# Optimization experiments

Hardware: AMD Instinct MI355X
Metric: run time of the kernel (lower is better)

Reference implementation:

```python
import jax, jax.numpy as jnp
import numpy as np

N = 200000
B = 2
GX, GY, GZ = 480, 360, 32          # full-res voxel grid for input_coords
GX2, GY2, GZ2 = 240, 180, 16       # output_scale grid for bxyz_indx
CIN, CR, COUT = 64, 64, 64
CR2 = CR // 2
P_SCALE = (2, 4, 6, 8)


def setup_inputs() -> dict:
    key = jax.random.key(0)
    ks = jax.random.split(key, 24)
    s = 0.05
    input_data = jax.random.normal(ks[0], (N, CIN), dtype=jnp.float32)
    bcol = jax.random.randint(ks[1], (N, 1), 0, B, dtype=jnp.int32)
    xc = jax.random.randint(ks[2], (N, 1), 0, GX, dtype=jnp.int32)
    yc = jax.random.randint(ks[3], (N, 1), 0, GY, dtype=jnp.int32)
    zc = jax.random.randint(ks[4], (N, 1), 0, GZ, dtype=jnp.int32)
    input_coords = jnp.concatenate([bcol, xc, yc, zc], axis=1)
    input_coords_inv = jax.random.randint(ks[5], (N,), 0, N, dtype=jnp.int32)
    b2 = jax.random.randint(ks[6], (N, 1), 0, B, dtype=jnp.int32)
    x2 = jax.random.randint(ks[7], (N, 1), 0, GX2, dtype=jnp.int32)
    y2 = jax.random.randint(ks[8], (N, 1), 0, GY2, dtype=jnp.int32)
    z2 = jax.random.randint(ks[9], (N, 1), 0, GZ2, dtype=jnp.int32)
    bxyz_indx = jnp.concatenate([b2, x2, y2, z2], axis=1)
    # parameters (torch Linear stored here as [in, out])
    W_red = jax.random.normal(ks[10], (CIN, CR)) * s
    b_red = jnp.zeros((CR,), jnp.float32)
    fc_list_W = jax.random.normal(ks[11], (4, CR, CR2)) * s
    fc_list_b = jnp.zeros((4, CR2), jnp.float32)
    fcs_W = jax.random.normal(ks[12], (4, CR2, CR2)) * s
    fcs_b = jnp.zeros((4, CR2), jnp.float32)
    fc_W = jax.random.normal(ks[13], (CR2, CR2)) * s
    out_fc_W = jax.random.normal(ks[14], (CR2, CR)) * s
    lo_W1 = jax.random.normal(ks[15], (2 * CR, CR)) * s
    lo_W2 = jax.random.normal(ks[16], (CR, COUT)) * s
    lo_b2 = jnp.zeros((COUT,), jnp.float32)
    return dict(input_data=input_data, input_coords=input_coords,
                input_coords_inv=input_coords_inv, bxyz_indx=bxyz_indx,
                W_red=W_red, b_red=b_red, fc_list_W=fc_list_W, fc_list_b=fc_list_b,
                fcs_W=fcs_W, fcs_b=fcs_b, fc_W=fc_W, out_fc_W=out_fc_W,
                lo_W1=lo_W1, lo_W2=lo_W2, lo_b2=lo_b2)


def _segment_mean(x, seg, num_segments):
    sums = jax.ops.segment_sum(x, seg, num_segments=num_segments)
    cnt = jax.ops.segment_sum(jnp.ones((x.shape[0], 1), x.dtype), seg,
                              num_segments=num_segments)
    return sums / jnp.maximum(cnt, 1.0)


def reference(input_data, input_coords, input_coords_inv, bxyz_indx,
              W_red, b_red, fc_list_W, fc_list_b, fcs_W, fcs_b,
              fc_W, out_fc_W, lo_W1, lo_W2, lo_b2):
    reduced = jax.nn.relu(input_data @ W_red + b_red)          # [N, CR]
    bcol = input_coords[:, 0]
    xyz = input_coords[:, 1:]
    outs = []
    for j, ps in enumerate(P_SCALE):
        dx = (GX - 1) // ps + 1
        dy = (GY - 1) // ps + 1
        dz = (GZ - 1) // ps + 1
        q = xyz // ps                                          # [N, 3]
        # dense linearized voxel id replaces torch.unique(return_inverse)
        lin = ((bcol * dx + q[:, 0]) * dy + q[:, 1]) * dz + q[:, 2]
        nseg = B * dx * dy * dz
        fkm = _segment_mean(reduced, lin, nseg)                # [nseg, CR]
        att = jax.nn.relu(fkm @ fc_list_W[j] + fc_list_b[j])   # [nseg, CR2]
        outs.append(att[lin])                                  # gather back [N, CR2]
    scale_features = jnp.stack(outs, axis=1)                   # [N, 4, CR2]
    feat_S = scale_features.sum(axis=1)                        # [N, CR2]
    feat_Z = jax.nn.relu(feat_S @ fc_W)                        # [N, CR2]
    att_v = jax.nn.sigmoid(jnp.einsum('nc,kcd->nkd', feat_Z, fcs_W) + fcs_b)
    fused = (scale_features * att_v).sum(axis=1) @ out_fc_W    # [N, CR]
    output_f = jnp.concatenate([reduced, fused], axis=1)       # [N, 2*CR]
    proj = jax.nn.relu(output_f @ lo_W1) @ lo_W2 + lo_b2       # [N, COUT]
    proj = proj[input_coords_inv]
    # with_fm branch: index = (b, z, y, x) of bxyz_indx (b,x,y,z)
    lin2 = ((bxyz_indx[:, 0] * GZ2 + bxyz_indx[:, 3]) * GY2
            + bxyz_indx[:, 2]) * GX2 + bxyz_indx[:, 1]
    tv_fmap = jax.ops.segment_max(proj, lin2, num_segments=B * GZ2 * GY2 * GX2)
    tv_fmap = jnp.where(jnp.isneginf(tv_fmap), 0.0, tv_fmap)   # empty voxels -> 0
    return proj, tv_fmap, lin2
```

## Files before the change

kernel.cpp:

```cpp
#include <hip/hip_runtime.h>
#include <math.h>

#define NPTS   200000
#define CR     64
#define CR2    32

#define NSEG0      1382400
#define SUM123_ROW2 172800
#define SUM123_ROW3 230400
#define SUM123_ROWS 252000

#define TVSEG  1382400
#define GX2    240
#define GY2    180
#define GZ2    16

#define NBATCH 21600

__device__ __forceinline__ float bcastf(float v, int l) {
    return __int_as_float(__builtin_amdgcn_readlane(__float_as_int(v), l));
}

__device__ __forceinline__ int lin_scale(int b, int x, int y, int z,
                                         int ps, int dx, int dy, int dz) {
    int qx = x / ps, qy = y / ps, qz = z / ps;
    return ((b * dx + qx) * dy + qy) * dz + qz;
}

__device__ __forceinline__ void seg_decode(int seg, int& l1, int& l2, int& l3) {
    int qz = seg & 15; int rest = seg >> 4;
    int qy = rest % 180; int rest2 = rest / 180;
    int qx = rest2 % 240; int bb = rest2 / 240;
    l1 = ((bb * 120 + (qx >> 1)) * 90 + (qy >> 1)) * 8 + (qz >> 1);
    l2 = ((bb *  80 + (qx / 3)) * 60 + (qy / 3)) * 6 + (qz / 3);
    l3 = ((bb *  60 + (qx >> 2)) * 45 + (qy >> 2)) * 4 + (qz >> 2);
}

__global__ __launch_bounds__(256) void k_redscat(
        const float* __restrict__ in, const int* __restrict__ coords,
        const float* __restrict__ Wred, const float* __restrict__ bred,
        float* __restrict__ red, float* __restrict__ sum0,
        float* __restrict__ cnt) {
    __shared__ float Wl[CR * CR];
    for (int i = threadIdx.x; i < CR * CR; i += blockDim.x) Wl[i] = Wred[i];
    __syncthreads();
    int lane = threadIdx.x & 63;
    float bl = bred[lane];
    int wid  = blockIdx.x * 4 + (threadIdx.x >> 6);
    int nw   = gridDim.x * 4;
    for (int p = wid; p < NPTS / 2; p += nw) {
        int r0 = 2 * p, r1 = r0 + 1;
        float x0 = in[(size_t)r0 * CR + lane];
        float x1 = in[(size_t)r1 * CR + lane];
        float acc0 = bl, acc1 = bl;
#pragma unroll
        for (int k = 0; k < CR; ++k) {
            float w = Wl[k * CR + lane];
            acc0 += bcastf(x0, k) * w;
            acc1 += bcastf(x1, k) * w;
        }
        acc0 = fmaxf(acc0, 0.f); acc1 = fmaxf(acc1, 0.f);
        red[(size_t)r0 * CR + lane] = acc0;
        red[(size_t)r1 * CR + lane] = acc1;
        int4 c0 = ((const int4*)coords)[r0];
        int4 c1 = ((const int4*)coords)[r1];
        int l0a = lin_scale(c0.x, c0.y, c0.z, c0.w, 2, 240, 180, 16);
        int l0b = lin_scale(c1.x, c1.y, c1.z, c1.w, 2, 240, 180, 16);
        atomicAdd(&sum0[(size_t)l0a * CR + lane], acc0);
        atomicAdd(&sum0[(size_t)l0b * CR + lane], acc1);
        if (lane == 0) {
            atomicAdd(&cnt[l0a], 1.0f);
            atomicAdd(&cnt[l0b], 1.0f);
        }
    }
}

__global__ __launch_bounds__(256) void k_buildlist(
        const float* __restrict__ cnt, int* __restrict__ list0,
        int* __restrict__ listCount, int* __restrict__ rankArr) {
    __shared__ int s_wavecnt[4];
    __shared__ int s_base;
    int lane = threadIdx.x & 63;
    int w = threadIdx.x >> 6;
    int batch0 = blockIdx.x * 80 + w * 20;
    int mycount = 0;
    for (int b = 0; b < 20; ++b) {
        float c = cnt[(batch0 + b) * 64 + lane];
        unsigned long long mask = __ballot(c > 0.f);
        mycount += __popcll(mask);
    }
    if (lane == 0) s_wavecnt[w] = mycount;
    __syncthreads();
    if (threadIdx.x == 0) {
        int tot = s_wavecnt[0] + s_wavecnt[1] + s_wavecnt[2] + s_wavecnt[3];
        s_base = atomicAdd(listCount, tot);
    }
    __syncthreads();
    int offset = s_base;
    for (int ww = 0; ww < w; ++ww) offset += s_wavecnt[ww];
    for (int b = 0; b < 20; ++b) {
        int cell = (batch0 + b) * 64 + lane;
        float c = cnt[cell];
        unsigned long long mask = __ballot(c > 0.f);
        if (c > 0.f) {
            int my = offset + __popcll(mask & ((1ull << lane) - 1ull));
            list0[my] = cell;
            rankArr[cell] = my;
        }
        offset += __popcll(mask);
    }
}

__global__ __launch_bounds__(256) void k_gatt(
        const float* __restrict__ sum0, float* __restrict__ attbuf,
        const float* __restrict__ cnt,
        const float* __restrict__ fcW, const float* __restrict__ fcB) {
    __shared__ float sw[3 * CR * CR2];
    for (int i = threadIdx.x; i < 3 * CR * CR2; i += blockDim.x)
        sw[i] = fcW[CR * CR2 + i];
    __syncthreads();
    int lane = threadIdx.x & 63;
    int d = lane & 31;
    int wid = blockIdx.x * 4 + (threadIdx.x >> 6);
    int nw  = gridDim.x * 4;
    for (int s = wid; s < SUM123_ROWS; s += nw) {
        int childLin = -1;
        const float* w; float bj;
        if (s < SUM123_ROW2) {
            int qz = s & 7, t = s >> 3;
            int qy = t % 90, t2 = t / 90;
            int qx = t2 % 120, b = t2 / 120;
            if (lane < 8) {
                int i = (lane >> 2) & 1, j = (lane >> 1) & 1, k = lane & 1;
                childLin = ((b * 240 + 2 * qx + i) * 180 + 2 * qy + j) * 16 + 2 * qz + k;
            }
            w = sw; bj = fcB[1 * CR2 + d];
        } else if (s < SUM123_ROW3) {
            int s2 = s - SUM123_ROW2;
            int qz = s2 % 6, t = s2 / 6;
            int qy = t % 60, t2 = t / 60;
            int qx = t2 % 80, b = t2 / 80;
            if (lane < 27) {
                int i = lane / 9, j = (lane / 3) % 3, k = lane % 3;
                int cz = 3 * qz + k;
                if (cz < 16)
                    childLin = ((b * 240 + 3 * qx + i) * 180 + 3 * qy + j) * 16 + cz;
            }
            w = sw + 2048; bj = fcB[2 * CR2 + d];
        } else {
            int s3 = s - SUM123_ROW3;
            int qz = s3 & 3, t = s3 >> 2;
            int qy = t % 45, t2 = t / 45;
            int qx = t2 % 60, b = t2 / 60;
            int i = lane >> 4, j = (lane >> 2) & 3, k = lane & 3;
            childLin = ((b * 240 + 4 * qx + i) * 180 + 4 * qy + j) * 16 + 4 * qz + k;
            w = sw + 4096; bj = fcB[3 * CR2 + d];
        }
        float myc = (childLin >= 0) ? cnt[childLin] : 0.f;
        unsigned long long mask = __ballot(myc > 0.f);
        if (!mask) continue;
        float ctot = myc;
        ctot += __shfl_xor(ctot, 1, 64);
        ctot += __shfl_xor(ctot, 2, 64);
        ctot += __shfl_xor(ctot, 4, 64);
        ctot += __shfl_xor(ctot, 8, 64);
        ctot += __shfl_xor(ctot, 16, 64);
        ctot += __shfl_xor(ctot, 32, 64);
        float acc = 0.f;
        while (mask) {
            int j = __ffsll((long long)mask) - 1; mask &= mask - 1;
            int cl = __builtin_amdgcn_readlane(childLin, j);
            acc += sum0[(size_t)cl * CR + lane];
        }
        float m = acc * (1.f / ctot);
        float p = bj;
#pragma unroll
        for (int k = 0; k < CR; ++k)
            p += bcastf(m, k) * w[k * CR2 + d];
        float att = fmaxf(p, 0.f);
        if (lane < 32) attbuf[(size_t)s * CR2 + lane] = att;
    }
}

__global__ __launch_bounds__(256) void k_att0z(
        float* __restrict__ tv, const float* __restrict__ cnt,
        const int* __restrict__ list0, const int* __restrict__ listCount,
        const float* __restrict__ fcW, const float* __restrict__ fcB,
        float* __restrict__ att0c) {
    __shared__ float sw[CR * CR2];
    for (int i = threadIdx.x; i < CR * CR2; i += blockDim.x) sw[i] = fcW[i];
    __syncthreads();
    int lane = threadIdx.x & 63;
    int d = lane & 31;
    int h = lane >> 5;
    float b0 = fcB[d];
    int total = listCount[0];
    int ngroups = (total + 3) >> 2;
    int wid = blockIdx.x * 4 + (threadIdx.x >> 6);
    int nw  = gridDim.x * 4;
    for (int g = wid; g < ngroups; g += nw) {
        int r0 = 4 * g;
        int r1 = min(r0 + 1, total - 1);
        int r2 = min(r0 + 2, total - 1);
        int r3 = min(r0 + 3, total - 1);
        int s0 = list0[r0], s1 = list0[r1], s2 = list0[r2], s3 = list0[r3];
        float* row0 = tv + (size_t)s0 * CR;
        float* row1 = tv + (size_t)s1 * CR;
        float* row2 = tv + (size_t)s2 * CR;
        float* row3 = tv + (size_t)s3 * CR;
        float m0 = row0[lane] * (1.f / cnt[s0]);
        float m1 = row1[lane] * (1.f / cnt[s1]);
        float m2 = row2[lane] * (1.f / cnt[s2]);
        float m3 = row3[lane] * (1.f / cnt[s3]);
        float p0 = b0, p1 = b0, p2 = b0, p3 = b0;
#pragma unroll
        for (int k = 0; k < CR; ++k) {
            float wk = sw[k * CR2 + d];
            p0 += bcastf(m0, k) * wk;
            p1 += bcastf(m1, k) * wk;
            p2 += bcastf(m2, k) * wk;
            p3 += bcastf(m3, k) * wk;
        }
        float a0 = fmaxf(p0, 0.f), a1 = fmaxf(p1, 0.f);
        float a2 = fmaxf(p2, 0.f), a3 = fmaxf(p3, 0.f);
        att0c[(size_t)(h ? r2 : r0) * CR2 + d] = h ? a2 : a0;
        att0c[(size_t)(h ? r3 : r1) * CR2 + d] = h ? a3 : a1;
        row0[lane] = 0.f; row1[lane] = 0.f; row2[lane] = 0.f; row3[lane] = 0.f;
    }
}

__global__ __launch_bounds__(1024) void k_mm(
        const float* __restrict__ outW, const float* __restrict__ loW1,
        float* __restrict__ M) {
    int e = threadIdx.x + blockIdx.x * 1024;
    if (e >= 2048) return;
    int r = e >> 6, c = e & 63;
    float acc = 0.f;
#pragma unroll
    for (int k = 0; k < 64; ++k)
        acc += outW[r * 64 + k] * loW1[(64 + k) * 64 + c];
    M[e] = acc;
}

__global__ __launch_bounds__(256) void k_seg(
        const int* __restrict__ list0, const int* __restrict__ listCount,
        const float* __restrict__ att0c, const float* __restrict__ attbuf,
        const float* __restrict__ fc_W, const float* __restrict__ fcsW,
        const float* __restrict__ fcsB, const float* __restrict__ M,
        float* __restrict__ gc) {
    __shared__ float s_fcZ[1024];
    __shared__ float s_fcs[4096];
    __shared__ float s_M[2048];
    for (int i = threadIdx.x; i < 1024; i += 256) s_fcZ[i]  = fc_W[i];
    for (int i = threadIdx.x; i < 4096; i += 256) s_fcs[i]  = fcsW[i];
    for (int i = threadIdx.x; i < 2048; i += 256) s_M[i]    = M[i];
    __syncthreads();

    int lane = threadIdx.x & 63;
    int d = lane & 31;
    int h = lane >> 5;
    float vbA = fcsB[(h ? 1 : 0) * CR2 + d];
    float vbB = fcsB[(h ? 3 : 2) * CR2 + d];
    const float* VA = s_fcs + (h ? 1 : 0) * 1024;
    const float* VB = s_fcs + (h ? 3 : 2) * 1024;

    int total = listCount[0];
    int ngroups = (total + 3) >> 2;
    int wid = blockIdx.x * 4 + (threadIdx.x >> 6);
    int nw  = gridDim.x * 4;
    for (int g = wid; g < ngroups; g += nw) {
        int r0 = 4 * g;
        int r1 = min(r0 + 1, total - 1);
        int r2 = min(r0 + 2, total - 1);
        int r3 = min(r0 + 3, total - 1);
        int seg0 = list0[r0], seg1 = list0[r1], seg2 = list0[r2], seg3 = list0[r3];

        int l1_0, l2_0, l3_0, l1_1, l2_1, l3_1;
        int l1_2, l2_2, l3_2, l1_3, l2_3, l3_3;
        seg_decode(seg0, l1_0, l2_0, l3_0);
        seg_decode(seg1, l1_1, l2_1, l3_1);
        seg_decode(seg2, l1_2, l2_2, l3_2);
        seg_decode(seg3, l1_3, l2_3, l3_3);

        float a0_0 = att0c[(size_t)r0 * CR2 + d];
        float a0_1 = att0c[(size_t)r1 * CR2 + d];
        float a0_2 = att0c[(size_t)r2 * CR2 + d];
        float a0_3 = att0c[(size_t)r3 * CR2 + d];
        float a1_0 = attbuf[(size_t)l1_0 * CR2 + d];
        float a2_0 = attbuf[(size_t)(SUM123_ROW2 + l2_0) * CR2 + d];
        float a3_0 = attbuf[(size_t)(SUM123_ROW3 + l3_0) * CR2 + d];
        float a1_1 = attbuf[(size_t)l1_1 * CR2 + d];
        float a2_1 = attbuf[(size_t)(SUM123_ROW2 + l2_1) * CR2 + d];
        float a3_1 = attbuf[(size_t)(SUM123_ROW3 + l3_1) * CR2 + d];
        float a1_2 = attbuf[(size_t)l1_2 * CR2 + d];
        float a2_2 = attbuf[(size_t)(SUM123_ROW2 + l2_2) * CR2 + d];
        float a3_2 = attbuf[(size_t)(SUM123_ROW3 + l3_2) * CR2 + d];
        float a1_3 = attbuf[(size_t)l1_3 * CR2 + d];
        float a2_3 = attbuf[(size_t)(SUM123_ROW2 + l2_3) * CR2 + d];
        float a3_3 = attbuf[(size_t)(SUM123_ROW3 + l3_3) * CR2 + d];

        float fS0 = a0_0 + a1_0 + a2_0 + a3_0;
        float fS1 = a0_1 + a1_1 + a2_1 + a3_1;
        float fS2 = a0_2 + a1_2 + a2_2 + a3_2;
        float fS3 = a0_3 + a1_3 + a2_3 + a3_3;

        float z0 = 0.f, z1 = 0.f, z2 = 0.f, z3 = 0.f;
#pragma unroll
        for (int cc = 0; cc < CR2; ++cc) {
            float wz = s_fcZ[cc * CR2 + d];
            z0 += bcastf(fS0, cc) * wz;
            z1 += bcastf(fS1, cc) * wz;
            z2 += bcastf(fS2, cc) * wz;
            z3 += bcastf(fS3, cc) * wz;
        }
        float fZ0 = fmaxf(z0, 0.f), fZ1 = fmaxf(z1, 0.f);
        float fZ2 = fmaxf(z2, 0.f), fZ3 = fmaxf(z3, 0.f);

        float avA0 = vbA, avA1 = vbA, avA2 = vbA, avA3 = vbA;
        float avB0 = vbB, avB1 = vbB, avB2 = vbB, avB3 = vbB;
#pragma unroll
        for (int cc = 0; cc < CR2; ++cc) {
            float wa = VA[cc * CR2 + d];
            float wb = VB[cc * CR2 + d];
            float f0 = bcastf(fZ0, cc), f1 = bcastf(fZ1, cc);
            float f2 = bcastf(fZ2, cc), f3 = bcastf(fZ3, cc);
            avA0 += f0 * wa; avB0 += f0 * wb;
            avA1 += f1 * wa; avB1 += f1 * wb;
            avA2 += f2 * wa; avB2 += f2 * wb;
            avA3 += f3 * wa; avB3 += f3 * wb;
        }
        avA0 = 1.f / (1.f + __expf(-avA0)); avB0 = 1.f / (1.f + __expf(-avB0));
        avA1 = 1.f / (1.f + __expf(-avA1)); avB1 = 1.f / (1.f + __expf(-avB1));
        avA2 = 1.f / (1.f + __expf(-avA2)); avB2 = 1.f / (1.f + __expf(-avB2));
        avA3 = 1.f / (1.f + __expf(-avA3)); avB3 = 1.f / (1.f + __expf(-avB3));

        float u0 = (h ? a1_0 : a0_0) * avA0 + (h ? a3_0 : a2_0) * avB0;
        float u1 = (h ? a1_1 : a0_1) * avA1 + (h ? a3_1 : a2_1) * avB1;
        float u2 = (h ? a1_2 : a0_2) * avA2 + (h ? a3_2 : a2_2) * avB2;
        float u3 = (h ? a1_3 : a0_3) * avA3 + (h ? a3_3 : a2_3) * avB3;
        float fI0 = u0 + __shfl_xor(u0, 32, 64);
        float fI1 = u1 + __shfl_xor(u1, 32, 64);
        float fI2 = u2 + __shfl_xor(u2, 32, 64);
        float fI3 = u3 + __shfl_xor(u3, 32, 64);

        float g0 = 0.f, g1 = 0.f, g2 = 0.f, g3 = 0.f;
#pragma unroll
        for (int dd = 0; dd < CR2; ++dd) {
            float wm = s_M[dd * CR + lane];
            g0 += bcastf(fI0, dd) * wm;
            g1 += bcastf(fI1, dd) * wm;
            g2 += bcastf(fI2, dd) * wm;
            g3 += bcastf(fI3, dd) * wm;
        }
        gc[(size_t)r0 * CR + lane] = g0;
        gc[(size_t)r1 * CR + lane] = g1;
        gc[(size_t)r2 * CR + lane] = g2;
        gc[(size_t)r3 * CR + lane] = g3;
    }
}

__device__ __forceinline__ unsigned int fkey(float f) {
    unsigned int b = __float_as_uint(f);
    return (b & 0x80000000u) ? ~b : (b | 0x80000000u);
}

__global__ __launch_bounds__(256) void k_pgmax(
        const float* __restrict__ red, const float* __restrict__ gc,
        const int* __restrict__ rankArr,
        const int* __restrict__ coords, const int* __restrict__ inv,
        const int* __restrict__ bxyz,
        const float* __restrict__ loW1, const float* __restrict__ loW2,
        const float* __restrict__ lob2, float* __restrict__ outProj,
        float* __restrict__ outLin, unsigned int* __restrict__ tvKey,
        unsigned char* __restrict__ flags) {
    __shared__ float s_W1[4096];
    __shared__ float s_W2[4096];
    for (int i = threadIdx.x; i < 4096; i += 256) s_W1[i] = loW1[i];
    for (int i = threadIdx.x; i < 4096; i += 256) s_W2[i] = loW2[i];
    __syncthreads();

    int lane = threadIdx.x & 63;
    float lob = lob2[lane];
    int wid = blockIdx.x * 4 + (threadIdx.x >> 6);
    int nw  = gridDim.x * 4;
    for (int q = wid; q < NPTS / 4; q += nw) {
        int i0 = 4 * q, i1 = i0 + 1, i2 = i0 + 2, i3 = i0 + 3;
        int s0 = inv[i0], s1 = inv[i1], s2 = inv[i2], s3 = inv[i3];
        int4 c0 = ((const int4*)coords)[s0];
        int4 c1 = ((const int4*)coords)[s1];
        int4 c2 = ((const int4*)coords)[s2];
        int4 c3 = ((const int4*)coords)[s3];
        int l0 = lin_scale(c0.x, c0.y, c0.z, c0.w, 2, 240, 180, 16);
        int l1 = lin_scale(c1.x, c1.y, c1.z, c1.w, 2, 240, 180, 16);
        int l2 = lin_scale(c2.x, c2.y, c2.z, c2.w, 2, 240, 180, 16);
        int l3 = lin_scale(c3.x, c3.y, c3.z, c3.w, 2, 240, 180, 16);
        int rk0 = rankArr[l0], rk1 = rankArr[l1];
        int rk2 = rankArr[l2], rk3 = rankArr[l3];

        float x0 = red[(size_t)s0 * CR + lane];
        float x1 = red[(size_t)s1 * CR + lane];
        float x2 = red[(size_t)s2 * CR + lane];
        float x3 = red[(size_t)s3 * CR + lane];
        float h0 = gc[(size_t)rk0 * CR + lane];
        float h1 = gc[(size_t)rk1 * CR + lane];
        float h2 = gc[(size_t)rk2 * CR + lane];
        float h3 = gc[(size_t)rk3 * CR + lane];
#pragma unroll
        for (int k = 0; k < CR; ++k) {
            float w = s_W1[k * CR + lane];
            h0 += bcastf(x0, k) * w;
            h1 += bcastf(x1, k) * w;
            h2 += bcastf(x2, k) * w;
            h3 += bcastf(x3, k) * w;
        }
        h0 = fmaxf(h0, 0.f); h1 = fmaxf(h1, 0.f);
        h2 = fmaxf(h2, 0.f); h3 = fmaxf(h3, 0.f);

        float q0 = lob, q1 = lob, q2 = lob, q3 = lob;
#pragma unroll
        for (int k = 0; k < CR; ++k) {
            float w = s_W2[k * CR + lane];
            q0 += bcastf(h0, k) * w;
            q1 += bcastf(h1, k) * w;
            q2 += bcastf(h2, k) * w;
            q3 += bcastf(h3, k) * w;
        }
        outProj[(size_t)i0 * CR + lane] = q0;
        outProj[(size_t)i1 * CR + lane] = q1;
        outProj[(size_t)i2 * CR + lane] = q2;
        outProj[(size_t)i3 * CR + lane] = q3;

        int4 b0 = ((const int4*)bxyz)[i0];
        int4 b1 = ((const int4*)bxyz)[i1];
        int4 b2 = ((const int4*)bxyz)[i2];
        int4 b3 = ((const int4*)bxyz)[i3];
        int n0 = ((b0.x * GZ2 + b0.w) * GY2 + b0.z) * GX2 + b0.y;
        int n1 = ((b1.x * GZ2 + b1.w) * GY2 + b1.z) * GX2 + b1.y;
        int n2 = ((b2.x * GZ2 + b2.w) * GY2 + b2.z) * GX2 + b2.y;
        int n3 = ((b3.x * GZ2 + b3.w) * GY2 + b3.z) * GX2 + b3.y;
        if (lane == 0) {
            outLin[i0] = (float)n0; flags[n0] = 1;
            outLin[i1] = (float)n1; flags[n1] = 1;
            outLin[i2] = (float)n2; flags[n2] = 1;
            outLin[i3] = (float)n3; flags[n3] = 1;
        }
        atomicMax(&tvKey[(size_t)n0 * CR + lane], fkey(q0));
        atomicMax(&tvKey[(size_t)n1 * CR + lane], fkey(q1));
        atomicMax(&tvKey[(size_t)n2 * CR + lane], fkey(q2));
        atomicMax(&tvKey[(size_t)n3 * CR + lane], fkey(q3));
    }
}

__global__ __launch_bounds__(256) void k_fix(
        unsigned int* __restrict__ tv, const unsigned char* __restrict__ flags) {
    int lane = threadIdx.x & 63;
    int wid = blockIdx.x * 4 + (threadIdx.x >> 6);
    int nw  = gridDim.x * 4;
    for (int batch = wid; batch < NBATCH; batch += nw) {
        int base = batch * 64;
        unsigned char f = flags[base + lane];
        unsigned long long mask = __ballot(f != 0);
        while (mask) {
            int j = __ffsll((long long)mask) - 1; mask &= mask - 1;
            size_t idx = (size_t)(base + j) * CR + lane;
            unsigned int k = tv[idx];
            float v = (k == 0u) ? 0.f
                    : __uint_as_float((k & 0x80000000u) ? (k & 0x7FFFFFFFu) : ~k);
            ((float*)tv)[idx] = v;
        }
    }
}

extern "C" void kernel_launch(void* const* d_in, const int* in_sizes, int n_in,
                              void* d_out, int out_size, void* d_ws, size_t ws_size,
                              hipStream_t stream) {
    (void)in_sizes; (void)n_in; (void)out_size; (void)ws_size;
    const float* in_data = (const float*)d_in[0];
    const int*   coords  = (const int*)d_in[1];
    const int*   inv     = (const int*)d_in[2];
    const int*   bxyz    = (const int*)d_in[3];
    const float* W_red   = (const float*)d_in[4];
    const float* b_red   = (const float*)d_in[5];
    const float* fcW     = (const float*)d_in[6];
    const float* fcB     = (const float*)d_in[7];
    const float* fcsW    = (const float*)d_in[8];
    const float* fcsB    = (const float*)d_in[9];
    const float* fc_W    = (const float*)d_in[10];
    const float* outW    = (const float*)d_in[11];
    const float* loW1    = (const float*)d_in[12];
    const float* loW2    = (const float*)d_in[13];
    const float* lob2    = (const float*)d_in[14];

    float* outProj = (float*)d_out;
    float* tv      = outProj + (size_t)NPTS * CR;
    float* outLin  = tv + (size_t)TVSEG * CR;

    float* ws_f   = (float*)d_ws;
    float* red    = ws_f;
    float* attbuf = red + (size_t)NPTS * CR;
    float* cnt    = attbuf + (size_t)SUM123_ROWS * CR2;
    int*   listCount = (int*)(cnt + (size_t)NSEG0);
    int*   rankArr   = listCount + 4;
    int*   list0     = rankArr + (size_t)NSEG0;
    float* att0c  = (float*)(list0 + (size_t)NPTS);
    float* gc     = att0c + (size_t)NPTS * CR2;
    float* Mmat   = gc + (size_t)NPTS * CR;
    unsigned char* flags = (unsigned char*)(Mmat + 2048);

    hipMemsetAsync(tv, 0, (size_t)TVSEG * CR * sizeof(float), stream);
    hipMemsetAsync(cnt, 0, ((size_t)NSEG0 + 4) * sizeof(float), stream);
    hipMemsetAsync(flags, 0, (size_t)TVSEG, stream);

    k_mm<<<2, 1024, 0, stream>>>(outW, loW1, Mmat);
    k_redscat<<<2048, 256, 0, stream>>>(in_data, coords, W_red, b_red,
                                        red, tv, cnt);
    k_buildlist<<<270, 256, 0, stream>>>(cnt, list0, (int*)listCount, rankArr);
    k_gatt<<<2048, 256, 0, stream>>>(tv, attbuf, cnt, fcW, fcB);
    k_att0z<<<1024, 256, 0, stream>>>(tv, cnt, list0, (const int*)listCount, fcW, fcB, att0c);
    k_seg<<<1024, 256, 0, stream>>>(list0, (const int*)listCount, att0c, attbuf,
                                    fc_W, fcsW, fcsB, Mmat, gc);
    k_pgmax<<<1024, 256, 0, stream>>>(red, gc, rankArr, coords, inv, bxyz,
                                      loW1, loW2, lob2, outProj,
                                      outLin, (unsigned int*)tv, flags);
    k_fix<<<512, 256, 0, stream>>>((unsigned int*)tv, flags);
}
```

Measured before the change: 1.043 ms.

## Fuse scale-0 attention into segment kernel and merge small launches

Merges k_att0z into k_seg as k_segf, so the scale-0 attention is computed in registers and the att0c round trip through global memory goes away. The k_mm weight product moves into extra blocks of k_buildlist, and the flags buffer is placed next to cnt so a single memset clears both, removing two launches and one memset. Grid sizes for k_pgmax and k_fix are doubled. The fused kernel holds more shared memory (about 36KB per block), which may lower occupancy.

```diff
diff --git a/kernel.cpp b/kernel.cpp
--- a/kernel.cpp
+++ b/kernel.cpp
@@ -77,7 +77,21 @@
 
 __global__ __launch_bounds__(256) void k_buildlist(
         const float* __restrict__ cnt, int* __restrict__ list0,
-        int* __restrict__ listCount, int* __restrict__ rankArr) {
+        int* __restrict__ listCount, int* __restrict__ rankArr,
+        const float* __restrict__ outW, const float* __restrict__ loW1,
+        float* __restrict__ M) {
+    if (blockIdx.x >= 270) {
+        int e = (blockIdx.x - 270) * 256 + threadIdx.x;
+        if (e < 2048) {
+            int r = e >> 6, c = e & 63;
+            float acc = 0.f;
+#pragma unroll
+            for (int k = 0; k < 64; ++k)
+                acc += outW[r * 64 + k] * loW1[(64 + k) * 64 + c];
+            M[e] = acc;
+        }
+        return;
+    }
     __shared__ int s_wavecnt[4];
     __shared__ int s_base;
     int lane = threadIdx.x & 63;
@@ -182,83 +196,27 @@
     }
 }
 
-__global__ __launch_bounds__(256) void k_att0z(
+__global__ __launch_bounds__(256) void k_segf(
         float* __restrict__ tv, const float* __restrict__ cnt,
         const int* __restrict__ list0, const int* __restrict__ listCount,
         const float* __restrict__ fcW, const float* __restrict__ fcB,
-        float* __restrict__ att0c) {
-    __shared__ float sw[CR * CR2];
-    for (int i = threadIdx.x; i < CR * CR2; i += blockDim.x) sw[i] = fcW[i];
-    __syncthreads();
-    int lane = threadIdx.x & 63;
-    int d = lane & 31;
-    int h = lane >> 5;
-    float b0 = fcB[d];
-    int total = listCount[0];
-    int ngroups = (total + 3) >> 2;
-    int wid = blockIdx.x * 4 + (threadIdx.x >> 6);
-    int nw  = gridDim.x * 4;
-    for (int g = wid; g < ngroups; g += nw) {
-        int r0 = 4 * g;
-        int r1 = min(r0 + 1, total - 1);
-        int r2 = min(r0 + 2, total - 1);
-        int r3 = min(r0 + 3, total - 1);
-        int s0 = list0[r0], s1 = list0[r1], s2 = list0[r2], s3 = list0[r3];
-        float* row0 = tv + (size_t)s0 * CR;
-        float* row1 = tv + (size_t)s1 * CR;
-        float* row2 = tv + (size_t)s2 * CR;
-        float* row3 = tv + (size_t)s3 * CR;
-        float m0 = row0[lane] * (1.f / cnt[s0]);
-        float m1 = row1[lane] * (1.f / cnt[s1]);
-        float m2 = row2[lane] * (1.f / cnt[s2]);
-        float m3 = row3[lane] * (1.f / cnt[s3]);
-        float p0 = b0, p1 = b0, p2 = b0, p3 = b0;
-#pragma unroll
-        for (int k = 0; k < CR; ++k) {
-            float wk = sw[k * CR2 + d];
-            p0 += bcastf(m0, k) * wk;
-            p1 += bcastf(m1, k) * wk;
-            p2 += bcastf(m2, k) * wk;
-            p3 += bcastf(m3, k) * wk;
-        }
-        float a0 = fmaxf(p0, 0.f), a1 = fmaxf(p1, 0.f);
-        float a2 = fmaxf(p2, 0.f), a3 = fmaxf(p3, 0.f);
-        att0c[(size_t)(h ? r2 : r0) * CR2 + d] = h ? a2 : a0;
-        att0c[(size_t)(h ? r3 : r1) * CR2 + d] = h ? a3 : a1;
-        row0[lane] = 0.f; row1[lane] = 0.f; row2[lane] = 0.f; row3[lane] = 0.f;
-    }
-}
-
-__global__ __launch_bounds__(1024) void k_mm(
-        const float* __restrict__ outW, const float* __restrict__ loW1,
-        float* __restrict__ M) {
-    int e = threadIdx.x + blockIdx.x * 1024;
-    if (e >= 2048) return;
-    int r = e >> 6, c = e & 63;
-    float acc = 0.f;
-#pragma unroll
-    for (int k = 0; k < 64; ++k)
-        acc += outW[r * 64 + k] * loW1[(64 + k) * 64 + c];
-    M[e] = acc;
-}
-
-__global__ __launch_bounds__(256) void k_seg(
-        const int* __restrict__ list0, const int* __restrict__ listCount,
-        const float* __restrict__ att0c, const float* __restrict__ attbuf,
         const float* __restrict__ fc_W, const float* __restrict__ fcsW,
         const float* __restrict__ fcsB, const float* __restrict__ M,
-        float* __restrict__ gc) {
+        const float* __restrict__ attbuf, float* __restrict__ gc) {
+    __shared__ float s_w0[2048];
     __shared__ float s_fcZ[1024];
     __shared__ float s_fcs[4096];
     __shared__ float s_M[2048];
-    for (int i = threadIdx.x; i < 1024; i += 256) s_fcZ[i]  = fc_W[i];
-    for (int i = threadIdx.x; i < 4096; i += 256) s_fcs[i]  = fcsW[i];
-    for (int i = threadIdx.x; i < 2048; i += 256) s_M[i]    = M[i];
+    for (int i = threadIdx.x; i < 2048; i += 256) s_w0[i]  = fcW[i];
+    for (int i = threadIdx.x; i < 1024; i += 256) s_fcZ[i] = fc_W[i];
+    for (int i = threadIdx.x; i < 4096; i += 256) s_fcs[i] = fcsW[i];
+    for (int i = threadIdx.x; i < 2048; i += 256) s_M[i]   = M[i];
     __syncthreads();
 
     int lane = threadIdx.x & 63;
     int d = lane & 31;
     int h = lane >> 5;
+    float b0  = fcB[d];
     float vbA = fcsB[(h ? 1 : 0) * CR2 + d];
     float vbB = fcsB[(h ? 3 : 2) * CR2 + d];
     const float* VA = s_fcs + (h ? 1 : 0) * 1024;
@@ -274,6 +232,27 @@
         int r2 = min(r0 + 2, total - 1);
         int r3 = min(r0 + 3, total - 1);
         int seg0 = list0[r0], seg1 = list0[r1], seg2 = list0[r2], seg3 = list0[r3];
+        float* row0 = tv + (size_t)seg0 * CR;
+        float* row1 = tv + (size_t)seg1 * CR;
+        float* row2 = tv + (size_t)seg2 * CR;
+        float* row3 = tv + (size_t)seg3 * CR;
+        float m0 = row0[lane] * (1.f / cnt[seg0]);
+        float m1 = row1[lane] * (1.f / cnt[seg1]);
+        float m2 = row2[lane] * (1.f / cnt[seg2]);
+        float m3 = row3[lane] * (1.f / cnt[seg3]);
+        row0[lane] = 0.f; row1[lane] = 0.f; row2[lane] = 0.f; row3[lane] = 0.f;
+
+        float p0 = b0, p1 = b0, p2 = b0, p3 = b0;
+#pragma unroll
+        for (int k = 0; k < CR; ++k) {
+            float wk = s_w0[k * CR2 + d];
+            p0 += bcastf(m0, k) * wk;
+            p1 += bcastf(m1, k) * wk;
+            p2 += bcastf(m2, k) * wk;
+            p3 += bcastf(m3, k) * wk;
+        }
+        float a0_0 = fmaxf(p0, 0.f), a0_1 = fmaxf(p1, 0.f);
+        float a0_2 = fmaxf(p2, 0.f), a0_3 = fmaxf(p3, 0.f);
 
         int l1_0, l2_0, l3_0, l1_1, l2_1, l3_1;
         int l1_2, l2_2, l3_2, l1_3, l2_3, l3_3;
@@ -282,10 +261,6 @@
         seg_decode(seg2, l1_2, l2_2, l3_2);
         seg_decode(seg3, l1_3, l2_3, l3_3);
 
-        float a0_0 = att0c[(size_t)r0 * CR2 + d];
-        float a0_1 = att0c[(size_t)r1 * CR2 + d];
-        float a0_2 = att0c[(size_t)r2 * CR2 + d];
-        float a0_3 = att0c[(size_t)r3 * CR2 + d];
         float a1_0 = attbuf[(size_t)l1_0 * CR2 + d];
         float a2_0 = attbuf[(size_t)(SUM123_ROW2 + l2_0) * CR2 + d];
         float a3_0 = attbuf[(size_t)(SUM123_ROW3 + l3_0) * CR2 + d];
@@ -500,27 +475,25 @@
     float* attbuf = red + (size_t)NPTS * CR;
     float* cnt    = attbuf + (size_t)SUM123_ROWS * CR2;
     int*   listCount = (int*)(cnt + (size_t)NSEG0);
-    int*   rankArr   = listCount + 4;
+    unsigned char* flags = (unsigned char*)(listCount + 4);
+    int*   rankArr   = (int*)(flags + (size_t)TVSEG);
     int*   list0     = rankArr + (size_t)NSEG0;
-    float* att0c  = (float*)(list0 + (size_t)NPTS);
-    float* gc     = att0c + (size_t)NPTS * CR2;
+    float* gc     = (float*)(list0 + (size_t)NPTS);
     float* Mmat   = gc + (size_t)NPTS * CR;
-    unsigned char* flags = (unsigned char*)(Mmat + 2048);
 
     hipMemsetAsync(tv, 0, (size_t)TVSEG * CR * sizeof(float), stream);
-    hipMemsetAsync(cnt, 0, ((size_t)NSEG0 + 4) * sizeof(float), stream);
-    hipMemsetAsync(flags, 0, (size_t)TVSEG, stream);
-
-    k_mm<<<2, 1024, 0, stream>>>(outW, loW1, Mmat);
+    hipMemsetAsync(cnt, 0, (size_t)NSEG0 * 4 + 16 + (size_t)TVSEG, stream);
+
     k_redscat<<<2048, 256, 0, stream>>>(in_data, coords, W_red, b_red,
                                         red, tv, cnt);
-    k_buildlist<<<270, 256, 0, stream>>>(cnt, list0, (int*)listCount, rankArr);
+    k_buildlist<<<278, 256, 0, stream>>>(cnt, list0, listCount, rankArr,
+                                         outW, loW1, Mmat);
     k_gatt<<<2048, 256, 0, stream>>>(tv, attbuf, cnt, fcW, fcB);
-    k_att0z<<<1024, 256, 0, stream>>>(tv, cnt, list0, (const int*)listCount, fcW, fcB, att0c);
-    k_seg<<<1024, 256, 0, stream>>>(list0, (const int*)listCount, att0c, attbuf,
-                                    fc_W, fcsW, fcsB, Mmat, gc);
-    k_pgmax<<<1024, 256, 0, stream>>>(red, gc, rankArr, coords, inv, bxyz,
+    k_segf<<<1024, 256, 0, stream>>>(tv, cnt, list0, (const int*)listCount,
+                                     fcW, fcB, fc_W, fcsW, fcsB, Mmat,
+                                     attbuf, gc);
+    k_pgmax<<<2048, 256, 0, stream>>>(red, gc, rankArr, coords, inv, bxyz,
                                       loW1, loW2, lob2, outProj,
                                       outLin, (unsigned int*)tv, flags);
-    k_fix<<<512, 256, 0, stream>>>((unsigned int*)tv, flags);
-}
+    k_fix<<<1024, 256, 0, stream>>>((unsigned int*)tv, flags);
+}
```

Result: faster. 1.005 ms (-3.6%).
